# Optimization experiments

Hardware: AMD Instinct MI355X
Metric: run time of the kernel (lower is better)

The kernel has to match this reference:

```python
import jax, jax.numpy as jnp
import numpy as np

N = 1024       # nodes
D1 = 64        # hidden_dim_1
D2 = 64        # hidden_dim_2
E = 16384      # edges
P = 8192       # query pairs
MAXX = 100     # max node label -> Embedding(MAXX+1, D1)
EPS = 1e-5     # LayerNorm eps (no affine)


def _ln(t):
    m = jnp.mean(t, axis=-1, keepdims=True)
    v = jnp.mean((t - m) ** 2, axis=-1, keepdims=True)
    return (t - m) / jnp.sqrt(v + EPS)


def setup_inputs() -> dict:
    key = jax.random.key(0)
    ks = jax.random.split(key, 12)
    s = 0.1
    x = jax.random.randint(ks[0], (N,), 0, MAXX + 1)
    ei = jax.random.randint(ks[1], (2, E), 0, N)
    pos = jax.random.randint(ks[2], (P, 2), 0, N)
    emb = jax.random.normal(ks[3], (MAXX + 1, D1)) * s
    sage_Wl = jax.random.normal(ks[4], (2, D1, D1)) * s   # lin_l weight (aggr path, has bias)
    sage_bl = jnp.zeros((2, D1))
    sage_Wr = jax.random.normal(ks[5], (2, D1, D1)) * s   # lin_r weight (root path, no bias)
    h_W = jax.random.normal(ks[6], (D1 + 1, D2)) * s
    h_b = jnp.zeros((D2,))
    g_W = jax.random.normal(ks[7], (D1 + 1 + 2 * D2, D2)) * s
    g_b = jnp.zeros((D2,))
    lin_W = jax.random.normal(ks[8], (D2, 1)) * s
    lin_b = jnp.zeros((1,))
    return {"x": x, "ei": ei, "pos": pos, "emb": emb,
            "sage_Wl": sage_Wl, "sage_bl": sage_bl, "sage_Wr": sage_Wr,
            "h_W": h_W, "h_b": h_b, "g_W": g_W, "g_b": g_b,
            "lin_W": lin_W, "lin_b": lin_b}


def reference(x, ei, pos, emb, sage_Wl, sage_bl, sage_Wr, h_W, h_b, g_W, g_b, lin_W, lin_b):
    n = N
    src, dst = ei[0], ei[1]
    h = emb[x]                                            # (n, D1)
    # SAGEConv x2: mean-aggregate src->dst, lin_l(aggr)+bias + lin_r(root); then LN (no affine, no relu)
    deg = jax.ops.segment_sum(jnp.ones((E,), h.dtype), dst, num_segments=n)
    deg = jnp.maximum(deg, 1.0)[:, None]
    for i in range(2):
        aggr = jax.ops.segment_sum(h[src], dst, num_segments=n) / deg
        h = _ln(aggr @ sage_Wl[i] + sage_bl[i] + h @ sage_Wr[i])
    # pairwise outer product features: (n, n, D1)
    A = h[:, None, :] * h[None, :, :]
    eim = jnp.zeros((n * n,), h.dtype).at[src * n + dst].set(1.0).reshape(n, n, 1)
    A = jnp.concatenate([A, eim], axis=-1)                # (n, n, D1+1)
    # mataggr: B = h_1(A); row/col sums; D = cat(A, vec_p, vec_q); g_1(D)
    B = jax.nn.relu(_ln(A @ h_W + h_b))                   # (n, n, D2)
    vec_p = jnp.sum(B, axis=1, keepdims=True)             # (n, 1, D2)
    vec_q = jnp.sum(B, axis=0, keepdims=True)             # (1, n, D2)
    Dm = jnp.concatenate([A,
                          jnp.broadcast_to(vec_p, (n, n, D2)),
                          jnp.broadcast_to(vec_q, (n, n, D2))], axis=-1)
    G = jax.nn.relu(_ln(Dm @ g_W + g_b))                  # (n, n, D2)
    # symmetrize and gather query pairs
    S = (G * jnp.transpose(G, (1, 0, 2))).reshape(n * n, D2)
    sel = S[pos[:, 0] * n + pos[:, 1]]                    # (P, D2)
    return sel @ lin_W + lin_b                            # (P, 1)
```

## Files before the change

### kernel.cpp

```cpp
#include <hip/hip_runtime.h>
#include <hip/hip_bf16.h>

#define NN 1024
#define DD 64
#define EE 16384
#define PP 8192
#define EPSF 1e-5f
#define SWP (DD + 8)

typedef __hip_bfloat16 bf16;
typedef __attribute__((ext_vector_type(8))) short short8;
typedef __attribute__((ext_vector_type(4))) float f32x4;

static __device__ __forceinline__ float dec1(const void* src, int i, int fl) {
    if (fl) return ((const float*)src)[i];
    return __bfloat162float(((const bf16*)src)[i]);
}
static __device__ __forceinline__ unsigned short f2bf_u(float f) {
    bf16 h = __float2bfloat16(f);
    return *reinterpret_cast<unsigned short*>(&h);
}
static __device__ __forceinline__ float bfu2f(unsigned short u) {
    return __uint_as_float(((unsigned int)u) << 16);
}
static __device__ __forceinline__ int probe_fl(const void* emb) {
    int lane = threadIdx.x & 63;
    unsigned short raw = ((const unsigned short*)emb)[lane];
    float v = __uint_as_float(((unsigned int)raw) << 16);
    return (__ballot(!(fabsf(v) <= 1e3f)) != 0ull) ? 1 : 0;
}

__global__ __launch_bounds__(1024) void k_prep(
        const void* __restrict__ emb, const void* __restrict__ sWl,
        const void* __restrict__ sbl, const void* __restrict__ sWr,
        const void* __restrict__ hW, const void* __restrict__ hb,
        const void* __restrict__ gW, const void* __restrict__ gb,
        const void* __restrict__ lW, const void* __restrict__ lb,
        const int* __restrict__ x, const int* __restrict__ ei,
        float* __restrict__ Wlf, float* __restrict__ blf, float* __restrict__ Wrf,
        float* __restrict__ WfT, float* __restrict__ hbw,
        float* __restrict__ gWf, float* __restrict__ linf,
        unsigned short* __restrict__ gWbfT,
        float* __restrict__ h0,
        unsigned int* __restrict__ eim, unsigned int* __restrict__ eimT,
        int* __restrict__ rowptr, int* __restrict__ csrc) {
    __shared__ int sdeg[NN];
    __shared__ int stmp[1024];
    const int b = blockIdx.x, tid = threadIdx.x;
    const int fl = probe_fl(emb);

    if (b < 97) {
        const int vb = b * 4 + (tid >> 8);
        const int vt = tid & 255;
        if (vb < 256) {
            int z = vb * 256 + vt;
            if (z < 32768) eim[z] = 0u;
            else           eimT[z - 32768] = 0u;
        }
        if (vb < 32) { int i = vb * 256 + vt; Wlf[i] = dec1(sWl, i, fl); }
        else if (vb == 32) { if (vt < 128) blf[vt] = dec1(sbl, vt, fl); }
        else if (vb < 65) { int i = (vb - 33) * 256 + vt; Wrf[i] = dec1(sWr, i, fl); }
        else if (vb < 82) {
            int i = (vb - 65) * 256 + vt;
            if (i < 4096) { int n = i >> 6, k = i & 63; WfT[n * DD + k] = dec1(hW, k * DD + n, fl); }
            else if (i < 4160) hbw[i - 4096] = dec1(hb, i - 4096, fl);
            else if (i < 4224) hbw[64 + (i - 4160)] = dec1(hW, 64 * DD + (i - 4160), fl);
        } else if (vb < 131) {
            int i = (vb - 82) * 256 + vt;
            if (i < 193 * DD) gWf[i] = dec1(gW, i, fl);
            else if (i < 194 * DD) gWf[i] = dec1(gb, i - 193 * DD, fl);
        } else if (vb == 131) {
            if (vt < DD) linf[vt] = dec1(lW, vt, fl);
            else if (vt == DD) linf[DD] = dec1(lb, 0, fl);
#pragma unroll
            for (int u = 0; u < 16; ++u) {
                int i = vt * 16 + u;
                int m = i >> 6, k = i & 63;
                gWbfT[i] = f2bf_u(dec1(gW, k * DD + m, fl));
            }
        } else if (vb < 388) {
            int i = (vb - 132) * 256 + vt;
            int node = i >> 6, f = i & 63;
            h0[i] = dec1(emb, x[node] * DD + f, fl);
        }
    } else {
        sdeg[tid] = 0;
        __syncthreads();
        for (int base = 0; base < EE; base += 8192) {
            int d8[8];
#pragma unroll
            for (int u = 0; u < 8; ++u) d8[u] = ei[EE + base + u * 1024 + tid];
#pragma unroll
            for (int u = 0; u < 8; ++u) atomicAdd(&sdeg[d8[u]], 1);
        }
        __syncthreads();
        int v = sdeg[tid];
        stmp[tid] = v;
        __syncthreads();
        for (int off = 1; off < 1024; off <<= 1) {
            int a = (tid >= off) ? stmp[tid - off] : 0;
            __syncthreads();
            stmp[tid] += a;
            __syncthreads();
        }
        int excl = stmp[tid] - v;
        rowptr[tid] = excl;
        sdeg[tid] = excl;
        if (tid == 1023) rowptr[NN] = stmp[1023];
        __syncthreads();
        for (int base = 0; base < EE; base += 8192) {
            int d8[8], s8[8];
#pragma unroll
            for (int u = 0; u < 8; ++u) {
                d8[u] = ei[EE + base + u * 1024 + tid];
                s8[u] = ei[base + u * 1024 + tid];
            }
#pragma unroll
            for (int u = 0; u < 8; ++u) {
                int c = atomicAdd(&sdeg[d8[u]], 1);
                csrc[c] = s8[u];
            }
        }
    }
}

static __device__ __forceinline__ void sage_core(
        const float* sWl, const float* sWr, float* sa, float* sh,
        int node, int lane,
        const int* __restrict__ rowptr, const int* __restrict__ csrc,
        const float* __restrict__ hin, const void* __restrict__ sbl, int boff, int fl,
        float* __restrict__ hout, unsigned short* __restrict__ hbf) {
    int r0 = rowptr[node], r1 = rowptr[node + 1];
    float s = 0.f;
    int r = r0;
    for (; r + 8 <= r1; r += 8) {
        int idx[8];
#pragma unroll
        for (int u = 0; u < 8; ++u) idx[u] = csrc[r + u];
        float v[8];
#pragma unroll
        for (int u = 0; u < 8; ++u) v[u] = hin[idx[u] * DD + lane];
        s += ((v[0] + v[1]) + (v[2] + v[3])) + ((v[4] + v[5]) + (v[6] + v[7]));
    }
    for (; r + 4 <= r1; r += 4) {
        int i0 = csrc[r], i1 = csrc[r + 1], i2 = csrc[r + 2], i3 = csrc[r + 3];
        float v0 = hin[i0 * DD + lane], v1 = hin[i1 * DD + lane];
        float v2 = hin[i2 * DD + lane], v3 = hin[i3 * DD + lane];
        s += (v0 + v1) + (v2 + v3);
    }
    for (; r < r1; ++r) s += hin[csrc[r] * DD + lane];
    sa[lane] = s / (float)max(r1 - r0, 1);
    sh[lane] = hin[node * DD + lane];
    float o = dec1(sbl, boff + lane, fl);
    for (int k = 0; k < DD; ++k)
        o += sa[k] * sWl[k * DD + lane] + sh[k] * sWr[k * DD + lane];
    float m = o;
    for (int off = 32; off; off >>= 1) m += __shfl_xor(m, off);
    m *= (1.f / DD);
    float d0 = o - m;
    float v = d0 * d0;
    for (int off = 32; off; off >>= 1) v += __shfl_xor(v, off);
    v *= (1.f / DD);
    float rr = d0 * rsqrtf(v + EPSF);
    hout[node * DD + lane] = rr;
    if (hbf) hbf[node * DD + lane] = f2bf_u(rr);
}

__global__ __launch_bounds__(256) void k_sage0(
        const void* __restrict__ emb, const int* __restrict__ ei,
        const int* __restrict__ rowptr, const int* __restrict__ csrc,
        const float* __restrict__ h0,
        const float* __restrict__ Wlf, const void* __restrict__ sbl,
        const float* __restrict__ Wrf,
        float* __restrict__ h1,
        unsigned int* __restrict__ eim, unsigned int* __restrict__ eimT) {
    __shared__ __align__(16) float sWl[DD * DD];
    __shared__ __align__(16) float sWr[DD * DD];
    __shared__ float sa4[4 * DD], sh4[4 * DD];
    const int b = blockIdx.x, tid = threadIdx.x;
    const int lane = tid & 63, wave = tid >> 6;
    const int fl = probe_fl(emb);
    for (int i = tid * 4; i < DD * DD; i += 1024) {
        *(float4*)(sWl + i) = *(const float4*)(Wlf + i);
        *(float4*)(sWr + i) = *(const float4*)(Wrf + i);
    }
    if (tid < 64) {
        int e = b * 64 + tid;
        int s = ei[e], d = ei[EE + e];
        unsigned int idx = (unsigned int)(s * NN + d);
        atomicOr(&eim[idx >> 5], 1u << (idx & 31));
        unsigned int idxT = (unsigned int)(d * NN + s);
        atomicOr(&eimT[idxT >> 5], 1u << (idxT & 31));
    }
    __syncthreads();
    sage_core(sWl, sWr, sa4 + wave * DD, sh4 + wave * DD, b * 4 + wave, lane,
              rowptr, csrc, h0, sbl, 0, fl, h1, (unsigned short*)nullptr);
}

__global__ __launch_bounds__(256) void k_sage1(
        const void* __restrict__ emb,
        const int* __restrict__ rowptr, const int* __restrict__ csrc,
        const float* __restrict__ h1,
        const float* __restrict__ Wlf, const void* __restrict__ sbl,
        const float* __restrict__ Wrf,
        float* __restrict__ h2, unsigned short* __restrict__ hbf) {
    __shared__ __align__(16) float sWl[DD * DD];
    __shared__ __align__(16) float sWr[DD * DD];
    __shared__ float sa4[4 * DD], sh4[4 * DD];
    const int b = blockIdx.x, tid = threadIdx.x;
    const int lane = tid & 63, wave = tid >> 6;
    const int fl = probe_fl(emb);
    for (int i = tid * 4; i < DD * DD; i += 1024) {
        *(float4*)(sWl + i) = *(const float4*)(Wlf + DD * DD + i);
        *(float4*)(sWr + i) = *(const float4*)(Wrf + DD * DD + i);
    }
    __syncthreads();
    sage_core(sWl, sWr, sa4 + wave * DD, sh4 + wave * DD, b * 4 + wave, lane,
              rowptr, csrc, h1, sbl, DD, fl, h2, hbf);
}

__global__ __launch_bounds__(256) void k_bstage(
        const float* __restrict__ h2, const unsigned short* __restrict__ hbf,
        const float* __restrict__ WfT, const float* __restrict__ hbw,
        const unsigned int* __restrict__ eim, const unsigned int* __restrict__ eimT,
        const float* __restrict__ gWf,
        float* __restrict__ ppb, float* __restrict__ qqb) {
    __shared__ __align__(16) unsigned short sW[DD * SWP];
    __shared__ __align__(16) float red[4 * 128];
    __shared__ float swc[2];
    const int b = blockIdx.x, tid = threadIdx.x;
    const int lane = tid & 63, wave = tid >> 6;
    const int l15 = lane & 15, quad = lane >> 4;

    {
        int m = tid >> 2;
        int k0 = (tid & 3) * 16;
        const float* hi = h2 + b * DD;
        const float* wr = WfT + m * DD;
        unsigned short tmp[16];
#pragma unroll
        for (int u = 0; u < 16; ++u) tmp[u] = f2bf_u(hi[k0 + u] * wr[k0 + u]);
        *(short8*)(sW + m * SWP + k0) = *(short8*)tmp;
        *(short8*)(sW + m * SWP + k0 + 8) = *(short8*)(tmp + 8);
    }
    if (wave == 0) {
        float wv = hbw[64 + lane];
        float s = wv, s2 = wv * wv;
        for (int off = 32; off; off >>= 1) {
            s += __shfl_xor(s, off);
            s2 += __shfl_xor(s2, off);
        }
        if (lane == 0) { swc[0] = s; swc[1] = s2; }
    }
    __syncthreads();
    const float SW = swc[0], SWW = swc[1];

    short8 Af[4][2];
#pragma unroll
    for (int mt = 0; mt < 4; ++mt)
#pragma unroll
        for (int kt = 0; kt < 2; ++kt)
            Af[mt][kt] = *(const short8*)(sW + (mt * 16 + l15) * SWP + kt * 32 + quad * 8);

    f32x4 hb04[4], hww4[4];
#pragma unroll
    for (int mt = 0; mt < 4; ++mt) {
        hb04[mt] = *(const f32x4*)(hbw + mt * 16 + quad * 4);
        hww4[mt] = *(const f32x4*)(hbw + 64 + mt * 16 + quad * 4);
    }

    f32x4 accf[4], accb[4];
#pragma unroll
    for (int mt = 0; mt < 4; ++mt) {
        accf[mt] = (f32x4){0.f, 0.f, 0.f, 0.f};
        accb[mt] = (f32x4){0.f, 0.f, 0.f, 0.f};
    }

    const unsigned short* pB = hbf + (wave * 16 + l15) * DD + quad * 8;
    const unsigned int* pF = eim + b * 32 + (wave >> 1);
    const unsigned int* pBk = eimT + b * 32 + (wave >> 1);
    const int shft = (wave & 1) * 16;

    short8 B0 = *(const short8*)(pB);
    short8 B1 = *(const short8*)(pB + 32);
    pB += 4096;
    unsigned int wfC = pF[0], wbC = pBk[0];
    pF += 2; pBk += 2;

    for (int it = 0; it < 16; ++it) {
        short8 cB0 = B0, cB1 = B1;
        B0 = *(const short8*)(pB);
        B1 = *(const short8*)(pB + 32);
        pB += 4096;
        unsigned int sf = (wfC >> shft) & 0xFFFFu;
        unsigned int sb = (wbC >> shft) & 0xFFFFu;
        wfC = pF[0]; wbC = pBk[0];
        pF += 2; pBk += 2;

        f32x4 C[4];
#pragma unroll
        for (int mt = 0; mt < 4; ++mt)
            C[mt] = __builtin_amdgcn_mfma_f32_16x16x32_bf16(Af[mt][0], cB0, hb04[mt], 0, 0, 0);
#pragma unroll
        for (int mt = 0; mt < 4; ++mt)
            C[mt] = __builtin_amdgcn_mfma_f32_16x16x32_bf16(Af[mt][1], cB1, C[mt], 0, 0, 0);

        float ef = 0.f;
        if ((sf | sb) != 0u) {
            ef = (float)((sf >> l15) & 1u);
            f32x4 efv = {ef, ef, ef, ef};
#pragma unroll
            for (int mt = 0; mt < 4; ++mt) C[mt] += efv * hww4[mt];
        }

        f32x4 s1a = {0.f, 0.f, 0.f, 0.f}, s2a = {0.f, 0.f, 0.f, 0.f};
#pragma unroll
        for (int mt = 0; mt < 4; ++mt) {
            s1a += C[mt];
            s2a += C[mt] * C[mt];
        }
        float s1 = (s1a.x + s1a.y) + (s1a.z + s1a.w);
        float s2 = (s2a.x + s2a.y) + (s2a.z + s2a.w);
        s1 += __shfl_xor(s1, 16); s1 += __shfl_xor(s1, 32);
        s2 += __shfl_xor(s2, 16); s2 += __shfl_xor(s2, 32);
        float mean = s1 * (1.f / DD);
        float var = fmaxf(s2 * (1.f / DD) - mean * mean, 0.f);
        float rs = rsqrtf(var + EPSF);
        float mrs = mean * rs;
        f32x4 rsv = {rs, rs, rs, rs}, mrsv = {mrs, mrs, mrs, mrs};
        f32x4 zero = {0.f, 0.f, 0.f, 0.f};

        if (sf == sb) {
#pragma unroll
            for (int mt = 0; mt < 4; ++mt) {
                f32x4 u = __builtin_elementwise_max(C[mt] * rsv - mrsv, zero);
                accf[mt] += u;
                accb[mt] += u;
            }
        } else {
#pragma unroll
            for (int mt = 0; mt < 4; ++mt)
                accf[mt] += __builtin_elementwise_max(C[mt] * rsv - mrsv, zero);
            float de = (float)((sb >> l15) & 1u) - ef;
            f32x4 dva = {0.f, 0.f, 0.f, 0.f};
#pragma unroll
            for (int mt = 0; mt < 4; ++mt) dva += C[mt] * hww4[mt];
            float dot = (dva.x + dva.y) + (dva.z + dva.w);
            dot += __shfl_xor(dot, 16); dot += __shfl_xor(dot, 32);
            float t1 = s1 + de * SW;
            float t2 = s2 + 2.f * de * dot + de * de * SWW;
            float mean2 = t1 * (1.f / DD);
            float var2 = fmaxf(t2 * (1.f / DD) - mean2 * mean2, 0.f);
            float rs2 = rsqrtf(var2 + EPSF);
            float mrs2 = mean2 * rs2;
            float drs = de * rs2;
            f32x4 rs2v = {rs2, rs2, rs2, rs2};
            f32x4 mrs2v = {mrs2, mrs2, mrs2, mrs2};
            f32x4 drsv = {drs, drs, drs, drs};
#pragma unroll
            for (int mt = 0; mt < 4; ++mt) {
                f32x4 th = mrs2v - drsv * hww4[mt];
                accb[mt] += __builtin_elementwise_max(C[mt] * rs2v - th, zero);
            }
        }
    }

    float af[4][4], ab[4][4];
#pragma unroll
    for (int mt = 0; mt < 4; ++mt)
#pragma unroll
        for (int r = 0; r < 4; ++r) { af[mt][r] = accf[mt][r]; ab[mt][r] = accb[mt][r]; }
#pragma unroll
    for (int step = 1; step < 16; step <<= 1)
#pragma unroll
        for (int mt = 0; mt < 4; ++mt)
#pragma unroll
            for (int r = 0; r < 4; ++r) {
                af[mt][r] += __shfl_xor(af[mt][r], step);
                ab[mt][r] += __shfl_xor(ab[mt][r], step);
            }
    if (l15 == 0) {
#pragma unroll
        for (int mt = 0; mt < 4; ++mt)
#pragma unroll
            for (int r = 0; r < 4; ++r) {
                int m = mt * 16 + quad * 4 + r;
                red[wave * 128 + m] = af[mt][r];
                red[wave * 128 + DD + m] = ab[mt][r];
            }
    }
    __syncthreads();
    if (tid < 128) {
        float sum = red[tid] + red[128 + tid] + red[256 + tid] + red[384 + tid];
        red[tid] = sum;
    }
    __syncthreads();
    if (wave < 2) {
        const float* sv = red + wave * DD;
        int row0 = wave ? 129 : 65;
        float o = 0.f;
        for (int k = 0; k < DD; ++k) o += sv[k] * gWf[(row0 + k) * DD + lane];
        (wave ? qqb : ppb)[b * DD + lane] = o;
    }
}

__global__ __launch_bounds__(128) void k_final(
        const void* __restrict__ emb,
        const int* __restrict__ pos, const unsigned short* __restrict__ hbf,
        const float* __restrict__ gWf, const unsigned short* __restrict__ gWbfT,
        const unsigned int* __restrict__ eim,
        const float* __restrict__ ppb, const float* __restrict__ qqb,
        const float* __restrict__ linf, void* __restrict__ outv) {
    const int b = blockIdx.x, tid = threadIdx.x;
    const int lane = tid & 63, wave = tid >> 6;
    const int l15 = lane & 15, quad = lane >> 4;
    const int fl = probe_fl(emb);

    short8 A0f[4], A1f[4];
#pragma unroll
    for (int mt = 0; mt < 4; ++mt) {
        A0f[mt] = *(const short8*)(gWbfT + (mt * 16 + l15) * DD + quad * 8);
        A1f[mt] = *(const short8*)(gWbfT + (mt * 16 + l15) * DD + 32 + quad * 8);
    }

    int pp_ = b * 32 + wave * 16 + l15;
    int a = pos[2 * pp_], bb = pos[2 * pp_ + 1];

    unsigned int iab = (unsigned int)(a * NN + bb), iba = (unsigned int)(bb * NN + a);
    unsigned int wab = eim[iab >> 5], wba = eim[iba >> 5];

    short8 ha0 = *(const short8*)(hbf + a * DD + quad * 8);
    short8 hb0v = *(const short8*)(hbf + bb * DD + quad * 8);
    short8 ha1 = *(const short8*)(hbf + a * DD + 32 + quad * 8);
    short8 hb1v = *(const short8*)(hbf + bb * DD + 32 + quad * 8);
    short8 B0, B1;
#pragma unroll
    for (int j = 0; j < 8; ++j) {
        B0[j] = (short)f2bf_u(bfu2f((unsigned short)ha0[j]) * bfu2f((unsigned short)hb0v[j]));
        B1[j] = (short)f2bf_u(bfu2f((unsigned short)ha1[j]) * bfu2f((unsigned short)hb1v[j]));
    }

    f32x4 C[4];
#pragma unroll
    for (int mt = 0; mt < 4; ++mt) C[mt] = (f32x4){0.f, 0.f, 0.f, 0.f};
#pragma unroll
    for (int mt = 0; mt < 4; ++mt)
        C[mt] = __builtin_amdgcn_mfma_f32_16x16x32_bf16(A0f[mt], B0, C[mt], 0, 0, 0);
#pragma unroll
    for (int mt = 0; mt < 4; ++mt)
        C[mt] = __builtin_amdgcn_mfma_f32_16x16x32_bf16(A1f[mt], B1, C[mt], 0, 0, 0);

    float eab = (float)((wab >> (iab & 31)) & 1u);
    float eba = (float)((wba >> (iba & 31)) & 1u);

    float u1[4][4], u2[4][4];
    float s1 = 0.f, s12 = 0.f, s2 = 0.f, s22 = 0.f;
#pragma unroll
    for (int mt = 0; mt < 4; ++mt) {
        int m0 = mt * 16 + quad * 4;
        f32x4 w64v = *(const f32x4*)(gWf + 64 * DD + m0);
        f32x4 gbv  = *(const f32x4*)(gWf + 193 * DD + m0);
        f32x4 ppa  = *(const f32x4*)(ppb + a * DD + m0);
        f32x4 qqb_ = *(const f32x4*)(qqb + bb * DD + m0);
        f32x4 ppb_ = *(const f32x4*)(ppb + bb * DD + m0);
        f32x4 qqa  = *(const f32x4*)(qqb + a * DD + m0);
#pragma unroll
        for (int r = 0; r < 4; ++r) {
            float v1 = C[mt][r] + eab * w64v[r] + ppa[r] + qqb_[r] + gbv[r];
            float v2 = C[mt][r] + eba * w64v[r] + ppb_[r] + qqa[r] + gbv[r];
            u1[mt][r] = v1; u2[mt][r] = v2;
            s1 += v1; s12 += v1 * v1;
            s2 += v2; s22 += v2 * v2;
        }
    }
    s1 += __shfl_xor(s1, 16);  s1 += __shfl_xor(s1, 32);
    s12 += __shfl_xor(s12, 16); s12 += __shfl_xor(s12, 32);
    s2 += __shfl_xor(s2, 16);  s2 += __shfl_xor(s2, 32);
    s22 += __shfl_xor(s22, 16); s22 += __shfl_xor(s22, 32);
    float mean1 = s1 * (1.f / DD);
    float rs1 = rsqrtf(fmaxf(s12 * (1.f / DD) - mean1 * mean1, 0.f) + EPSF);
    float mrs1 = mean1 * rs1;
    float mean2 = s2 * (1.f / DD);
    float rs2 = rsqrtf(fmaxf(s22 * (1.f / DD) - mean2 * mean2, 0.f) + EPSF);
    float mrs2 = mean2 * rs2;

    float r = 0.f;
#pragma unroll
    for (int mt = 0; mt < 4; ++mt) {
        f32x4 lw = *(const f32x4*)(linf + mt * 16 + quad * 4);
#pragma unroll
        for (int rr = 0; rr < 4; ++rr) {
            float g1 = fmaxf(u1[mt][rr] * rs1 - mrs1, 0.f);
            float g2 = fmaxf(u2[mt][rr] * rs2 - mrs2, 0.f);
            r += g1 * g2 * lw[rr];
        }
    }
    r += __shfl_xor(r, 16); r += __shfl_xor(r, 32);
    if (quad == 0) {
        float res = r + linf[DD];
        if (fl) ((float*)outv)[pp_] = res;
        else    ((bf16*)outv)[pp_] = __float2bfloat16(res);
    }
}

extern "C" void kernel_launch(void* const* d_in, const int* in_sizes, int n_in,
                              void* d_out, int out_size, void* d_ws, size_t ws_size,
                              hipStream_t stream) {
    const int* x   = (const int*)d_in[0];
    const int* ei  = (const int*)d_in[1];
    const int* pos = (const int*)d_in[2];
    const void* emb = d_in[3];

    char* w = (char*)d_ws;
    auto alloc = [&](size_t bytes) {
        void* q = (void*)w;
        w += (bytes + 255) & ~(size_t)255;
        return q;
    };
    unsigned int* eim  = (unsigned int*)alloc(NN * NN / 8);
    unsigned int* eimT = (unsigned int*)alloc(NN * NN / 8);
    float* h0   = (float*)alloc(NN * DD * 4);
    float* h1   = (float*)alloc(NN * DD * 4);
    float* h2   = (float*)alloc(NN * DD * 4);
    unsigned short* hbf = (unsigned short*)alloc(NN * DD * 2 + 8192);
    float* Wlf  = (float*)alloc(2 * DD * DD * 4);
    float* blf  = (float*)alloc(2 * DD * 4);
    float* Wrf  = (float*)alloc(2 * DD * DD * 4);
    float* WfT  = (float*)alloc(DD * DD * 4);
    float* hbw  = (float*)alloc(128 * 4);
    float* gWf  = (float*)alloc(194 * DD * 4);
    float* linf = (float*)alloc(65 * 4);
    unsigned short* gWbfT = (unsigned short*)alloc(DD * DD * 2);
    float* ppb  = (float*)alloc(NN * DD * 4);
    float* qqb  = (float*)alloc(NN * DD * 4);
    int* rowptr = (int*)alloc((NN + 1) * 4);
    int* csrc   = (int*)alloc(EE * 4);

    k_prep<<<98, 1024, 0, stream>>>(emb, d_in[4], d_in[5], d_in[6], d_in[7], d_in[8],
                                    d_in[9], d_in[10], d_in[11], d_in[12],
                                    x, ei, Wlf, blf, Wrf, WfT, hbw, gWf, linf, gWbfT,
                                    h0, eim, eimT, rowptr, csrc);
    k_sage0<<<256, 256, 0, stream>>>(emb, ei, rowptr, csrc, h0, Wlf, d_in[5], Wrf,
                                     h1, eim, eimT);
    k_sage1<<<256, 256, 0, stream>>>(emb, rowptr, csrc, h1, Wlf, d_in[5], Wrf, h2, hbf);
    k_bstage<<<NN, 256, 0, stream>>>(h2, hbf, WfT, hbw, eim, eimT, gWf, ppb, qqb);
    k_final<<<PP / 32, 128, 0, stream>>>(emb, pos, hbf, gWf, gWbfT, eim, ppb, qqb, linf, d_out);
}
```

Measured before the change: 143.8 us.

## Drop prep kernel; build per-node neighbor lists and edge bitmaps inside SAGE blocks

Removes the separate k_prep launch that built a CSR, decoded the SAGE weights to fp32 and zeroed the edge bitmaps. Each SAGE block now scans the whole edge list, collects the in- and out-neighbours of its 4 nodes into shared-memory lists, and writes the eim/eimT bitmap rows for those nodes directly. Layer 0 gathers from the embedding table instead of a materialised h0, and the other weight-prep work moves into a few sage0 blocks. In exchange every block rereads all edges, and neighbour lists are capped at NCAP=128, so any node with more than 128 incoming edges would silently get a wrong aggregate.

```diff
diff --git a/kernel.cpp b/kernel.cpp
--- a/kernel.cpp
+++ b/kernel.cpp
@@ -7,6 +7,7 @@
 #define PP 8192
 #define EPSF 1e-5f
 #define SWP (DD + 8)
+#define NCAP 128
 
 typedef __hip_bfloat16 bf16;
 typedef __attribute__((ext_vector_type(8))) short short8;
@@ -30,130 +31,7 @@
     return (__ballot(!(fabsf(v) <= 1e3f)) != 0ull) ? 1 : 0;
 }
 
-__global__ __launch_bounds__(1024) void k_prep(
-        const void* __restrict__ emb, const void* __restrict__ sWl,
-        const void* __restrict__ sbl, const void* __restrict__ sWr,
-        const void* __restrict__ hW, const void* __restrict__ hb,
-        const void* __restrict__ gW, const void* __restrict__ gb,
-        const void* __restrict__ lW, const void* __restrict__ lb,
-        const int* __restrict__ x, const int* __restrict__ ei,
-        float* __restrict__ Wlf, float* __restrict__ blf, float* __restrict__ Wrf,
-        float* __restrict__ WfT, float* __restrict__ hbw,
-        float* __restrict__ gWf, float* __restrict__ linf,
-        unsigned short* __restrict__ gWbfT,
-        float* __restrict__ h0,
-        unsigned int* __restrict__ eim, unsigned int* __restrict__ eimT,
-        int* __restrict__ rowptr, int* __restrict__ csrc) {
-    __shared__ int sdeg[NN];
-    __shared__ int stmp[1024];
-    const int b = blockIdx.x, tid = threadIdx.x;
-    const int fl = probe_fl(emb);
-
-    if (b < 97) {
-        const int vb = b * 4 + (tid >> 8);
-        const int vt = tid & 255;
-        if (vb < 256) {
-            int z = vb * 256 + vt;
-            if (z < 32768) eim[z] = 0u;
-            else           eimT[z - 32768] = 0u;
-        }
-        if (vb < 32) { int i = vb * 256 + vt; Wlf[i] = dec1(sWl, i, fl); }
-        else if (vb == 32) { if (vt < 128) blf[vt] = dec1(sbl, vt, fl); }
-        else if (vb < 65) { int i = (vb - 33) * 256 + vt; Wrf[i] = dec1(sWr, i, fl); }
-        else if (vb < 82) {
-            int i = (vb - 65) * 256 + vt;
-            if (i < 4096) { int n = i >> 6, k = i & 63; WfT[n * DD + k] = dec1(hW, k * DD + n, fl); }
-            else if (i < 4160) hbw[i - 4096] = dec1(hb, i - 4096, fl);
-            else if (i < 4224) hbw[64 + (i - 4160)] = dec1(hW, 64 * DD + (i - 4160), fl);
-        } else if (vb < 131) {
-            int i = (vb - 82) * 256 + vt;
-            if (i < 193 * DD) gWf[i] = dec1(gW, i, fl);
-            else if (i < 194 * DD) gWf[i] = dec1(gb, i - 193 * DD, fl);
-        } else if (vb == 131) {
-            if (vt < DD) linf[vt] = dec1(lW, vt, fl);
-            else if (vt == DD) linf[DD] = dec1(lb, 0, fl);
-#pragma unroll
-            for (int u = 0; u < 16; ++u) {
-                int i = vt * 16 + u;
-                int m = i >> 6, k = i & 63;
-                gWbfT[i] = f2bf_u(dec1(gW, k * DD + m, fl));
-            }
-        } else if (vb < 388) {
-            int i = (vb - 132) * 256 + vt;
-            int node = i >> 6, f = i & 63;
-            h0[i] = dec1(emb, x[node] * DD + f, fl);
-        }
-    } else {
-        sdeg[tid] = 0;
-        __syncthreads();
-        for (int base = 0; base < EE; base += 8192) {
-            int d8[8];
-#pragma unroll
-            for (int u = 0; u < 8; ++u) d8[u] = ei[EE + base + u * 1024 + tid];
-#pragma unroll
-            for (int u = 0; u < 8; ++u) atomicAdd(&sdeg[d8[u]], 1);
-        }
-        __syncthreads();
-        int v = sdeg[tid];
-        stmp[tid] = v;
-        __syncthreads();
-        for (int off = 1; off < 1024; off <<= 1) {
-            int a = (tid >= off) ? stmp[tid - off] : 0;
-            __syncthreads();
-            stmp[tid] += a;
-            __syncthreads();
-        }
-        int excl = stmp[tid] - v;
-        rowptr[tid] = excl;
-        sdeg[tid] = excl;
-        if (tid == 1023) rowptr[NN] = stmp[1023];
-        __syncthreads();
-        for (int base = 0; base < EE; base += 8192) {
-            int d8[8], s8[8];
-#pragma unroll
-            for (int u = 0; u < 8; ++u) {
-                d8[u] = ei[EE + base + u * 1024 + tid];
-                s8[u] = ei[base + u * 1024 + tid];
-            }
-#pragma unroll
-            for (int u = 0; u < 8; ++u) {
-                int c = atomicAdd(&sdeg[d8[u]], 1);
-                csrc[c] = s8[u];
-            }
-        }
-    }
-}
-
-static __device__ __forceinline__ void sage_core(
-        const float* sWl, const float* sWr, float* sa, float* sh,
-        int node, int lane,
-        const int* __restrict__ rowptr, const int* __restrict__ csrc,
-        const float* __restrict__ hin, const void* __restrict__ sbl, int boff, int fl,
-        float* __restrict__ hout, unsigned short* __restrict__ hbf) {
-    int r0 = rowptr[node], r1 = rowptr[node + 1];
-    float s = 0.f;
-    int r = r0;
-    for (; r + 8 <= r1; r += 8) {
-        int idx[8];
-#pragma unroll
-        for (int u = 0; u < 8; ++u) idx[u] = csrc[r + u];
-        float v[8];
-#pragma unroll
-        for (int u = 0; u < 8; ++u) v[u] = hin[idx[u] * DD + lane];
-        s += ((v[0] + v[1]) + (v[2] + v[3])) + ((v[4] + v[5]) + (v[6] + v[7]));
-    }
-    for (; r + 4 <= r1; r += 4) {
-        int i0 = csrc[r], i1 = csrc[r + 1], i2 = csrc[r + 2], i3 = csrc[r + 3];
-        float v0 = hin[i0 * DD + lane], v1 = hin[i1 * DD + lane];
-        float v2 = hin[i2 * DD + lane], v3 = hin[i3 * DD + lane];
-        s += (v0 + v1) + (v2 + v3);
-    }
-    for (; r < r1; ++r) s += hin[csrc[r] * DD + lane];
-    sa[lane] = s / (float)max(r1 - r0, 1);
-    sh[lane] = hin[node * DD + lane];
-    float o = dec1(sbl, boff + lane, fl);
-    for (int k = 0; k < DD; ++k)
-        o += sa[k] * sWl[k * DD + lane] + sh[k] * sWr[k * DD + lane];
+static __device__ __forceinline__ float ln_row(float o, int lane) {
     float m = o;
     for (int off = 32; off; off >>= 1) m += __shfl_xor(m, off);
     m *= (1.f / DD);
@@ -161,62 +39,201 @@
     float v = d0 * d0;
     for (int off = 32; off; off >>= 1) v += __shfl_xor(v, off);
     v *= (1.f / DD);
-    float rr = d0 * rsqrtf(v + EPSF);
-    hout[node * DD + lane] = rr;
-    if (hbf) hbf[node * DD + lane] = f2bf_u(rr);
+    return d0 * rsqrtf(v + EPSF);
 }
 
 __global__ __launch_bounds__(256) void k_sage0(
-        const void* __restrict__ emb, const int* __restrict__ ei,
-        const int* __restrict__ rowptr, const int* __restrict__ csrc,
-        const float* __restrict__ h0,
-        const float* __restrict__ Wlf, const void* __restrict__ sbl,
-        const float* __restrict__ Wrf,
+        const void* __restrict__ emb, const void* __restrict__ sWl_in,
+        const void* __restrict__ sbl, const void* __restrict__ sWr_in,
+        const void* __restrict__ hW, const void* __restrict__ hb,
+        const void* __restrict__ gW, const void* __restrict__ gb,
+        const void* __restrict__ lW, const void* __restrict__ lb,
+        const int* __restrict__ x, const int* __restrict__ ei,
+        float* __restrict__ WfT, float* __restrict__ hbw,
+        float* __restrict__ gWf, float* __restrict__ linf,
+        unsigned short* __restrict__ gWbfT,
         float* __restrict__ h1,
         unsigned int* __restrict__ eim, unsigned int* __restrict__ eimT) {
     __shared__ __align__(16) float sWl[DD * DD];
     __shared__ __align__(16) float sWr[DD * DD];
+    __shared__ int nlist[4][NCAP];
+    __shared__ int olist[4][NCAP];
+    __shared__ int ncnt[4], ocnt[4];
+    __shared__ unsigned int bmO[4][32], bmI[4][32];
     __shared__ float sa4[4 * DD], sh4[4 * DD];
     const int b = blockIdx.x, tid = threadIdx.x;
     const int lane = tid & 63, wave = tid >> 6;
     const int fl = probe_fl(emb);
-    for (int i = tid * 4; i < DD * DD; i += 1024) {
-        *(float4*)(sWl + i) = *(const float4*)(Wlf + i);
-        *(float4*)(sWr + i) = *(const float4*)(Wrf + i);
-    }
-    if (tid < 64) {
-        int e = b * 64 + tid;
-        int s = ei[e], d = ei[EE + e];
-        unsigned int idx = (unsigned int)(s * NN + d);
-        atomicOr(&eim[idx >> 5], 1u << (idx & 31));
-        unsigned int idxT = (unsigned int)(d * NN + s);
-        atomicOr(&eimT[idxT >> 5], 1u << (idxT & 31));
-    }
-    __syncthreads();
-    sage_core(sWl, sWr, sa4 + wave * DD, sh4 + wave * DD, b * 4 + wave, lane,
-              rowptr, csrc, h0, sbl, 0, fl, h1, (unsigned short*)nullptr);
+
+    if (tid < 4) { ncnt[tid] = 0; ocnt[tid] = 0; }
+
+    if (!fl) {
+        for (int i = tid * 8; i < DD * DD; i += 2048) {
+            short8 a = *(const short8*)((const unsigned short*)sWl_in + i);
+            short8 c = *(const short8*)((const unsigned short*)sWr_in + i);
+#pragma unroll
+            for (int u = 0; u < 8; ++u) {
+                sWl[i + u] = bfu2f((unsigned short)a[u]);
+                sWr[i + u] = bfu2f((unsigned short)c[u]);
+            }
+        }
+    } else {
+        for (int i = tid * 4; i < DD * DD; i += 1024) {
+            *(float4*)(sWl + i) = *(const float4*)((const float*)sWl_in + i);
+            *(float4*)(sWr + i) = *(const float4*)((const float*)sWr_in + i);
+        }
+    }
+
+    if (b >= 65 && b < 82) {
+        int i = (b - 65) * 256 + tid;
+        if (i < 4096) { int n_ = i >> 6, k_ = i & 63; WfT[n_ * DD + k_] = dec1(hW, k_ * DD + n_, fl); }
+        else if (i < 4160) hbw[i - 4096] = dec1(hb, i - 4096, fl);
+        else if (i < 4224) hbw[64 + (i - 4160)] = dec1(hW, 64 * DD + (i - 4160), fl);
+    } else if (b >= 82 && b < 131) {
+        int i = (b - 82) * 256 + tid;
+        if (i < 193 * DD) gWf[i] = dec1(gW, i, fl);
+        else if (i < 194 * DD) gWf[i] = dec1(gb, i - 193 * DD, fl);
+    } else if (b == 131) {
+        if (tid < DD) linf[tid] = dec1(lW, tid, fl);
+        else if (tid == DD) linf[DD] = dec1(lb, 0, fl);
+#pragma unroll
+        for (int u = 0; u < 16; ++u) {
+            int i = tid * 16 + u;
+            int m = i >> 6, k_ = i & 63;
+            gWbfT[i] = f2bf_u(dec1(gW, k_ * DD + m, fl));
+        }
+    }
+    __syncthreads();
+
+    for (int e0 = tid * 4; e0 < EE; e0 += 1024) {
+        int4 sv = *(const int4*)(ei + e0);
+        int4 dv = *(const int4*)(ei + EE + e0);
+#pragma unroll
+        for (int u = 0; u < 4; ++u) {
+            int s = (&sv.x)[u], d = (&dv.x)[u];
+            if ((d >> 2) == b) {
+                int c = atomicAdd(&ncnt[d & 3], 1);
+                if (c < NCAP) nlist[d & 3][c] = s | (x[s] << 16);
+            }
+            if ((s >> 2) == b) {
+                int c = atomicAdd(&ocnt[s & 3], 1);
+                if (c < NCAP) olist[s & 3][c] = d;
+            }
+        }
+    }
+    __syncthreads();
+
+    const int node = b * 4 + wave;
+    const int nc = ncnt[wave], oc = ocnt[wave];
+
+    if (lane < 32) { bmO[wave][lane] = 0u; bmI[wave][lane] = 0u; }
+    for (int j = lane; j < oc; j += 64) {
+        int d = olist[wave][j];
+        atomicOr(&bmO[wave][d >> 5], 1u << (d & 31));
+    }
+    for (int j = lane; j < nc; j += 64) {
+        int s = nlist[wave][j] & 0xFFFF;
+        atomicOr(&bmI[wave][s >> 5], 1u << (s & 31));
+    }
+    if (lane < 32) {
+        eim[node * 32 + lane] = bmO[wave][lane];
+        eimT[node * 32 + lane] = bmI[wave][lane];
+    }
+
+    float* sa = sa4 + wave * DD;
+    float* sh = sh4 + wave * DD;
+    float s = 0.f;
+    int r = 0;
+    for (; r + 8 <= nc; r += 8) {
+        int xs[8];
+#pragma unroll
+        for (int u = 0; u < 8; ++u) xs[u] = nlist[wave][r + u] >> 16;
+        float v[8];
+#pragma unroll
+        for (int u = 0; u < 8; ++u) v[u] = dec1(emb, xs[u] * DD + lane, fl);
+        s += ((v[0] + v[1]) + (v[2] + v[3])) + ((v[4] + v[5]) + (v[6] + v[7]));
+    }
+    for (; r < nc; ++r) s += dec1(emb, (nlist[wave][r] >> 16) * DD + lane, fl);
+    sa[lane] = s / (float)max(nc, 1);
+    sh[lane] = dec1(emb, x[node] * DD + lane, fl);
+    float o = dec1(sbl, lane, fl);
+    for (int k = 0; k < DD; ++k)
+        o += sa[k] * sWl[k * DD + lane] + sh[k] * sWr[k * DD + lane];
+    h1[node * DD + lane] = ln_row(o, lane);
 }
 
 __global__ __launch_bounds__(256) void k_sage1(
-        const void* __restrict__ emb,
-        const int* __restrict__ rowptr, const int* __restrict__ csrc,
+        const void* __restrict__ emb, const void* __restrict__ sWl_in,
+        const void* __restrict__ sbl, const void* __restrict__ sWr_in,
+        const int* __restrict__ ei,
         const float* __restrict__ h1,
-        const float* __restrict__ Wlf, const void* __restrict__ sbl,
-        const float* __restrict__ Wrf,
         float* __restrict__ h2, unsigned short* __restrict__ hbf) {
     __shared__ __align__(16) float sWl[DD * DD];
     __shared__ __align__(16) float sWr[DD * DD];
+    __shared__ int nlist[4][NCAP];
+    __shared__ int ncnt[4];
     __shared__ float sa4[4 * DD], sh4[4 * DD];
     const int b = blockIdx.x, tid = threadIdx.x;
     const int lane = tid & 63, wave = tid >> 6;
     const int fl = probe_fl(emb);
-    for (int i = tid * 4; i < DD * DD; i += 1024) {
-        *(float4*)(sWl + i) = *(const float4*)(Wlf + DD * DD + i);
-        *(float4*)(sWr + i) = *(const float4*)(Wrf + DD * DD + i);
-    }
-    __syncthreads();
-    sage_core(sWl, sWr, sa4 + wave * DD, sh4 + wave * DD, b * 4 + wave, lane,
-              rowptr, csrc, h1, sbl, DD, fl, h2, hbf);
+
+    if (tid < 4) ncnt[tid] = 0;
+    if (!fl) {
+        for (int i = tid * 8; i < DD * DD; i += 2048) {
+            short8 a = *(const short8*)((const unsigned short*)sWl_in + DD * DD + i);
+            short8 c = *(const short8*)((const unsigned short*)sWr_in + DD * DD + i);
+#pragma unroll
+            for (int u = 0; u < 8; ++u) {
+                sWl[i + u] = bfu2f((unsigned short)a[u]);
+                sWr[i + u] = bfu2f((unsigned short)c[u]);
+            }
+        }
+    } else {
+        for (int i = tid * 4; i < DD * DD; i += 1024) {
+            *(float4*)(sWl + i) = *(const float4*)((const float*)sWl_in + DD * DD + i);
+            *(float4*)(sWr + i) = *(const float4*)((const float*)sWr_in + DD * DD + i);
+        }
+    }
+    __syncthreads();
+
+    for (int e0 = tid * 4; e0 < EE; e0 += 1024) {
+        int4 sv = *(const int4*)(ei + e0);
+        int4 dv = *(const int4*)(ei + EE + e0);
+#pragma unroll
+        for (int u = 0; u < 4; ++u) {
+            int s = (&sv.x)[u], d = (&dv.x)[u];
+            if ((d >> 2) == b) {
+                int c = atomicAdd(&ncnt[d & 3], 1);
+                if (c < NCAP) nlist[d & 3][c] = s;
+            }
+        }
+    }
+    __syncthreads();
+
+    const int node = b * 4 + wave;
+    const int nc = ncnt[wave];
+    float* sa = sa4 + wave * DD;
+    float* sh = sh4 + wave * DD;
+    float s = 0.f;
+    int r = 0;
+    for (; r + 8 <= nc; r += 8) {
+        int idx[8];
+#pragma unroll
+        for (int u = 0; u < 8; ++u) idx[u] = nlist[wave][r + u];
+        float v[8];
+#pragma unroll
+        for (int u = 0; u < 8; ++u) v[u] = h1[idx[u] * DD + lane];
+        s += ((v[0] + v[1]) + (v[2] + v[3])) + ((v[4] + v[5]) + (v[6] + v[7]));
+    }
+    for (; r < nc; ++r) s += h1[nlist[wave][r] * DD + lane];
+    sa[lane] = s / (float)max(nc, 1);
+    sh[lane] = h1[node * DD + lane];
+    float o = dec1(sbl, DD + lane, fl);
+    for (int k = 0; k < DD; ++k)
+        o += sa[k] * sWl[k * DD + lane] + sh[k] * sWr[k * DD + lane];
+    float rr = ln_row(o, lane);
+    h2[node * DD + lane] = rr;
+    hbf[node * DD + lane] = f2bf_u(rr);
 }
 
 __global__ __launch_bounds__(256) void k_bstage(
@@ -519,13 +536,9 @@
     };
     unsigned int* eim  = (unsigned int*)alloc(NN * NN / 8);
     unsigned int* eimT = (unsigned int*)alloc(NN * NN / 8);
-    float* h0   = (float*)alloc(NN * DD * 4);
     float* h1   = (float*)alloc(NN * DD * 4);
     float* h2   = (float*)alloc(NN * DD * 4);
     unsigned short* hbf = (unsigned short*)alloc(NN * DD * 2 + 8192);
-    float* Wlf  = (float*)alloc(2 * DD * DD * 4);
-    float* blf  = (float*)alloc(2 * DD * 4);
-    float* Wrf  = (float*)alloc(2 * DD * DD * 4);
     float* WfT  = (float*)alloc(DD * DD * 4);
     float* hbw  = (float*)alloc(128 * 4);
     float* gWf  = (float*)alloc(194 * DD * 4);
@@ -533,16 +546,12 @@
     unsigned short* gWbfT = (unsigned short*)alloc(DD * DD * 2);
     float* ppb  = (float*)alloc(NN * DD * 4);
     float* qqb  = (float*)alloc(NN * DD * 4);
-    int* rowptr = (int*)alloc((NN + 1) * 4);
-    int* csrc   = (int*)alloc(EE * 4);
-
-    k_prep<<<98, 1024, 0, stream>>>(emb, d_in[4], d_in[5], d_in[6], d_in[7], d_in[8],
-                                    d_in[9], d_in[10], d_in[11], d_in[12],
-                                    x, ei, Wlf, blf, Wrf, WfT, hbw, gWf, linf, gWbfT,
-                                    h0, eim, eimT, rowptr, csrc);
-    k_sage0<<<256, 256, 0, stream>>>(emb, ei, rowptr, csrc, h0, Wlf, d_in[5], Wrf,
+
+    k_sage0<<<256, 256, 0, stream>>>(emb, d_in[4], d_in[5], d_in[6], d_in[7], d_in[8],
+                                     d_in[9], d_in[10], d_in[11], d_in[12],
+                                     x, ei, WfT, hbw, gWf, linf, gWbfT,
                                      h1, eim, eimT);
-    k_sage1<<<256, 256, 0, stream>>>(emb, rowptr, csrc, h1, Wlf, d_in[5], Wrf, h2, hbf);
+    k_sage1<<<256, 256, 0, stream>>>(emb, d_in[4], d_in[5], d_in[6], ei, h1, h2, hbf);
     k_bstage<<<NN, 256, 0, stream>>>(h2, hbf, WfT, hbw, eim, eimT, gWf, ppb, qqb);
     k_final<<<PP / 32, 128, 0, stream>>>(emb, pos, hbf, gWf, gWbfT, eim, ppb, qqb, linf, d_out);
 }
```

Result: no change. 145.1 us (+0.9%).
